# Optimization experiments

Hardware: AMD Instinct MI355X
Metric: run time of the kernel (lower is better)

## Reference

```python
import jax, jax.numpy as jnp
import numpy as np

BLOCK = 64
# Standard NF4 codebook (bitsandbytes), 16 quantile-based values in [-1, 1].
NF4_CODEBOOK = jnp.array([
    -1.0, -0.6961928009986877, -0.5250730514526367, -0.39491748809814453,
    -0.28444138169288635, -0.18477343022823334, -0.09105003625154495, 0.0,
    0.07958029955625534, 0.16093020141124725, 0.24611230194568634,
    0.33791524171829224, 0.44070982933044434, 0.5626170039176941,
    0.6848514676094055, 1.0], dtype=jnp.float32)


def dequantize_nf4(codes, absmax, shape):
    # codes: int array of 4-bit indices (unpacked), absmax: one scale per BLOCK.
    vals = NF4_CODEBOOK[codes.reshape(-1)]              # [N]
    vals = vals.reshape(-1, BLOCK) * absmax[:, None]    # blockwise rescale
    return vals.reshape(shape)


def setup_inputs() -> dict:
    key = jax.random.key(0)
    k1, k2, k3, k4, k5 = jax.random.split(key, 5)
    B, S, D_IN, D_OUT = 4, 2048, 4096, 4096
    x = jax.random.normal(k1, (B, S, D_IN), dtype=jnp.float32)
    w_codes = jax.random.randint(k2, (D_OUT, D_IN), 0, 16, dtype=jnp.int32)
    w_absmax = jax.random.uniform(k3, (D_OUT * D_IN // BLOCK,), dtype=jnp.float32)
    b_codes = jax.random.randint(k4, (D_OUT,), 0, 16, dtype=jnp.int32)
    b_absmax = jax.random.uniform(k5, (D_OUT // BLOCK,), dtype=jnp.float32)
    return {"x": x, "w_codes": w_codes, "w_absmax": w_absmax,
            "b_codes": b_codes, "b_absmax": b_absmax}


def reference(x, w_codes, w_absmax, b_codes, b_absmax):
    W = dequantize_nf4(w_codes, w_absmax, w_codes.shape)   # [out, in]
    b = dequantize_nf4(b_codes, b_absmax, b_codes.shape)   # [out]
    # F.linear(x, W, b) = x @ W.T + b
    return jnp.einsum('bsd,od->bso', x, W) + b
```

## Files before the change

kernel.cpp:

```cpp
#include <hip/hip_runtime.h>
#include <stdint.h>

typedef __bf16 bf16_t;
typedef __attribute__((ext_vector_type(8))) __bf16 bf16x8;
typedef __attribute__((ext_vector_type(4))) float f32x4;
typedef __attribute__((ext_vector_type(8))) unsigned short ushort8;
typedef __attribute__((ext_vector_type(4))) int int4v;
typedef __attribute__((ext_vector_type(4))) float float4v;

typedef const void __attribute__((address_space(1)))* gptr_t;
typedef void __attribute__((address_space(3)))* lptr_t;

__constant__ float NF4_CB[16] = {
    -1.0f, -0.6961928009986877f, -0.5250730514526367f, -0.39491748809814453f,
    -0.28444138169288635f, -0.18477343022823334f, -0.09105003625154495f, 0.0f,
    0.07958029955625534f, 0.16093020141124725f, 0.24611230194568634f,
    0.33791524171829224f, 0.44070982933044434f, 0.5626170039176941f,
    0.6848514676094055f, 1.0f};

__device__ __forceinline__ unsigned short f32_to_bf16_rne(float f) {
    unsigned int u = __float_as_uint(f);
    u += 0x7FFFu + ((u >> 16) & 1u);
    return (unsigned short)(u >> 16);
}

__global__ void prep_kernel(const int* __restrict__ w_codes,
                            const float* __restrict__ w_absmax,
                            const float* __restrict__ x,
                            const int* __restrict__ b_codes,
                            const float* __restrict__ b_absmax,
                            unsigned short* __restrict__ outW,
                            unsigned short* __restrict__ outA,
                            float* __restrict__ outBias,
                            long w16, long x16, int nbias, long wb, long xb) {
    __shared__ float cb[16];
    if (threadIdx.x < 16) cb[threadIdx.x] = NF4_CB[threadIdx.x];
    __syncthreads();

    long blk = blockIdx.x;
    if (blk < wb) {
        long t = blk * blockDim.x + threadIdx.x;
        if (t >= w16) return;
        long base = t * 16;
        float am = w_absmax[t >> 2];
        int4v c0 = *(const int4v*)(w_codes + base);
        int4v c1 = *(const int4v*)(w_codes + base + 4);
        int4v c2 = *(const int4v*)(w_codes + base + 8);
        int4v c3 = *(const int4v*)(w_codes + base + 12);
        ushort8 v0, v1;
        v0[0] = f32_to_bf16_rne(cb[c0[0]] * am);
        v0[1] = f32_to_bf16_rne(cb[c0[1]] * am);
        v0[2] = f32_to_bf16_rne(cb[c0[2]] * am);
        v0[3] = f32_to_bf16_rne(cb[c0[3]] * am);
        v0[4] = f32_to_bf16_rne(cb[c1[0]] * am);
        v0[5] = f32_to_bf16_rne(cb[c1[1]] * am);
        v0[6] = f32_to_bf16_rne(cb[c1[2]] * am);
        v0[7] = f32_to_bf16_rne(cb[c1[3]] * am);
        v1[0] = f32_to_bf16_rne(cb[c2[0]] * am);
        v1[1] = f32_to_bf16_rne(cb[c2[1]] * am);
        v1[2] = f32_to_bf16_rne(cb[c2[2]] * am);
        v1[3] = f32_to_bf16_rne(cb[c2[3]] * am);
        v1[4] = f32_to_bf16_rne(cb[c3[0]] * am);
        v1[5] = f32_to_bf16_rne(cb[c3[1]] * am);
        v1[6] = f32_to_bf16_rne(cb[c3[2]] * am);
        v1[7] = f32_to_bf16_rne(cb[c3[3]] * am);
        *(ushort8*)(outW + base) = v0;
        *(ushort8*)(outW + base + 8) = v1;
    } else if (blk < wb + xb) {
        long t = (blk - wb) * blockDim.x + threadIdx.x;
        if (t >= x16) return;
        long base = t * 16;
        float4v f0 = *(const float4v*)(x + base);
        float4v f1 = *(const float4v*)(x + base + 4);
        float4v f2 = *(const float4v*)(x + base + 8);
        float4v f3 = *(const float4v*)(x + base + 12);
        ushort8 v0, v1;
        v0[0] = f32_to_bf16_rne(f0[0]);
        v0[1] = f32_to_bf16_rne(f0[1]);
        v0[2] = f32_to_bf16_rne(f0[2]);
        v0[3] = f32_to_bf16_rne(f0[3]);
        v0[4] = f32_to_bf16_rne(f1[0]);
        v0[5] = f32_to_bf16_rne(f1[1]);
        v0[6] = f32_to_bf16_rne(f1[2]);
        v0[7] = f32_to_bf16_rne(f1[3]);
        v1[0] = f32_to_bf16_rne(f2[0]);
        v1[1] = f32_to_bf16_rne(f2[1]);
        v1[2] = f32_to_bf16_rne(f2[2]);
        v1[3] = f32_to_bf16_rne(f2[3]);
        v1[4] = f32_to_bf16_rne(f3[0]);
        v1[5] = f32_to_bf16_rne(f3[1]);
        v1[6] = f32_to_bf16_rne(f3[2]);
        v1[7] = f32_to_bf16_rne(f3[3]);
        *(ushort8*)(outA + base) = v0;
        *(ushort8*)(outA + base + 8) = v1;
    } else {
        int o = (int)(blk - wb - xb) * blockDim.x + threadIdx.x;
        if (o >= nbias) return;
        outBias[o] = cb[b_codes[o]] * b_absmax[o >> 6];
    }
}

__global__ __launch_bounds__(512, 2) void gemm_bias_kernel_256x256(
        const bf16_t* __restrict__ A, const bf16_t* __restrict__ B,
        const float* __restrict__ bias, float* __restrict__ C,
        int M, int N, int K) {
    __shared__ __align__(16) bf16_t sAB[65536];

    const int t = threadIdx.x;
    const int lane = t & 63;
    const int wave = t >> 6;

    const int nbx = gridDim.x;
    const int nwg = nbx * (int)gridDim.y;
    int flat = (int)blockIdx.y * nbx + (int)blockIdx.x;
    if ((nwg & 7) == 0) flat = (flat & 7) * (nwg >> 3) + (flat >> 3);
    const int tileM = (flat / nbx) * 256;
    const int tileN = (flat % nbx) * 256;

    const int rloc = lane >> 3;
    const int jsw  = (lane & 7) ^ rloc;
    const bf16_t* srcp[8];
#pragma unroll
    for (int j = 0; j < 8; ++j) {
        int c = wave * 8 + j;
        int isB = c >> 5;
        int r = (c & 31) * 8 + rloc;
        const bf16_t* base = isB ? (B + (size_t)(tileN + r) * K)
                                 : (A + (size_t)(tileM + r) * K);
        srcp[j] = base + jsw * 8;
    }
    bf16_t* dst0 = &sAB[wave * 4096 + lane * 8];

    auto stage = [&](int bufsel) {
        bf16_t* d = dst0 + bufsel * 32768;
#pragma unroll
        for (int j = 0; j < 8; ++j) {
            __builtin_amdgcn_global_load_lds((gptr_t)srcp[j],
                                             (lptr_t)(d + j * 512), 16, 0, 0);
            srcp[j] += 64;
        }
    };

    const int wm = wave >> 2;
    const int wn = wave & 3;
    const int la = lane & 15;
    const int jA = lane >> 4;
    const int jj0 = (jA ^ (lane & 7)) * 8;
    const int aoff = (wm * 128 + la) * 64 + jj0;
    const int boff = 16384 + (wn * 64 + la) * 64 + jj0;

    f32x4 acc[8][4] = {};
    const int nt = K >> 6;

    stage(0);
    stage(1);
    asm volatile("s_waitcnt vmcnt(8)" ::: "memory");
    __builtin_amdgcn_s_barrier();
    asm volatile("" ::: "memory");

    for (int kt = 0; kt < nt; ++kt) {
        const int base = (kt & 1) << 15;
#pragma unroll
        for (int kh = 0; kh < 2; ++kh) {
            const int kx = kh << 5;
            bf16x8 a[4], b[4];
#pragma unroll
            for (int i = 0; i < 4; ++i)
                b[i] = *(const bf16x8*)&sAB[((boff + i * 1024) ^ kx) + base];
#pragma unroll
            for (int i = 0; i < 4; ++i)
                a[i] = *(const bf16x8*)&sAB[((aoff + i * 1024) ^ kx) + base];
            __builtin_amdgcn_s_setprio(1);
#pragma unroll
            for (int mi = 0; mi < 4; ++mi)
#pragma unroll
                for (int ni = 0; ni < 4; ++ni)
                    acc[mi][ni] = __builtin_amdgcn_mfma_f32_16x16x32_bf16(
                        a[mi], b[ni], acc[mi][ni], 0, 0, 0);
            __builtin_amdgcn_s_setprio(0);
#pragma unroll
            for (int i = 0; i < 4; ++i)
                a[i] = *(const bf16x8*)&sAB[((aoff + (i + 4) * 1024) ^ kx) + base];
            __builtin_amdgcn_s_setprio(1);
#pragma unroll
            for (int mi = 0; mi < 4; ++mi)
#pragma unroll
                for (int ni = 0; ni < 4; ++ni)
                    acc[mi + 4][ni] = __builtin_amdgcn_mfma_f32_16x16x32_bf16(
                        a[mi], b[ni], acc[mi + 4][ni], 0, 0, 0);
            __builtin_amdgcn_s_setprio(0);
        }
        asm volatile("" ::: "memory");
        __builtin_amdgcn_s_barrier();
        if (kt + 2 < nt) {
            stage(kt & 1);
            asm volatile("s_waitcnt vmcnt(8)" ::: "memory");
        } else {
            asm volatile("s_waitcnt vmcnt(0)" ::: "memory");
        }
        __builtin_amdgcn_s_barrier();
        asm volatile("" ::: "memory");
    }

    const int col0 = tileN + wn * 64 + la;
    const int row0 = tileM + wm * 128 + jA * 4;
    float bv[4];
#pragma unroll
    for (int ni = 0; ni < 4; ++ni) bv[ni] = bias[col0 + ni * 16];
#pragma unroll
    for (int mi = 0; mi < 8; ++mi)
#pragma unroll
        for (int ni = 0; ni < 4; ++ni)
#pragma unroll
            for (int r = 0; r < 4; ++r)
                C[(size_t)(row0 + mi * 16 + r) * N + (col0 + ni * 16)] =
                    acc[mi][ni][r] + bv[ni];
}

__global__ __launch_bounds__(512) void gemm_bias_kernel_256(
        const bf16_t* __restrict__ A, const bf16_t* __restrict__ B,
        const float* __restrict__ bias, float* __restrict__ C,
        int M, int N, int K) {
    __shared__ __align__(16) bf16_t sAB[24576];

    const int t = threadIdx.x;
    const int lane = t & 63;
    const int wave = t >> 6;
    const int tileM = blockIdx.y * 256;
    const int tileN = blockIdx.x * 128;

    const int rloc = lane >> 3;
    const int jsw  = (lane & 7) ^ rloc;
    const bf16_t* srcp[6];
    bf16_t* dstp[6];
#pragma unroll
    for (int j = 0; j < 6; ++j) {
        int c = wave * 6 + j;
        int isB = (c >= 32);
        int r = (isB ? (c - 32) : c) * 8 + rloc;
        const bf16_t* base = isB ? (B + (size_t)(tileN + r) * K)
                                 : (A + (size_t)(tileM + r) * K);
        srcp[j] = base + jsw * 8;
        dstp[j] = &sAB[c * 512 + lane * 8];
    }

    const int wm = wave >> 1;
    const int wn = wave & 1;
    const int la = lane & 15;
    const int jA = lane >> 4;
    const int jj0 = (jA ^ (lane & 7)) * 8;
    const int aoff = (wm * 64 + la) * 64 + jj0;
    const int boff = 16384 + (wn * 64 + la) * 64 + jj0;

    f32x4 acc[4][4] = {};

    for (int kt = 0; kt < K; kt += 64) {
#pragma unroll
        for (int j = 0; j < 6; ++j) {
            __builtin_amdgcn_global_load_lds((gptr_t)(srcp[j]), (lptr_t)(dstp[j]),
                                             16, 0, 0);
            srcp[j] += 64;
        }
        __syncthreads();

#pragma unroll
        for (int kh = 0; kh < 2; ++kh) {
            const int kx = kh * 32;
            bf16x8 a[4], b[4];
#pragma unroll
            for (int i = 0; i < 4; ++i) a[i] = *(const bf16x8*)&sAB[(aoff + i * 1024) ^ kx];
#pragma unroll
            for (int i = 0; i < 4; ++i) b[i] = *(const bf16x8*)&sAB[(boff + i * 1024) ^ kx];
#pragma unroll
            for (int mi = 0; mi < 4; ++mi)
#pragma unroll
                for (int ni = 0; ni < 4; ++ni)
                    acc[mi][ni] = __builtin_amdgcn_mfma_f32_16x16x32_bf16(
                        a[mi], b[ni], acc[mi][ni], 0, 0, 0);
        }
        __syncthreads();
    }

    const int col0 = tileN + wn * 64 + la;
    const int row0 = tileM + wm * 64 + jA * 4;
    float bv[4];
#pragma unroll
    for (int ni = 0; ni < 4; ++ni) bv[ni] = bias[col0 + ni * 16];
#pragma unroll
    for (int mi = 0; mi < 4; ++mi)
#pragma unroll
        for (int ni = 0; ni < 4; ++ni)
#pragma unroll
            for (int r = 0; r < 4; ++r)
                C[(size_t)(row0 + mi * 16 + r) * N + (col0 + ni * 16)] =
                    acc[mi][ni][r] + bv[ni];
}

__global__ void gemm_bias_kernel_128(const bf16_t* __restrict__ A,
                                     const bf16_t* __restrict__ B,
                                     const float* __restrict__ bias,
                                     float* __restrict__ C,
                                     int M, int N, int K) {
    __shared__ __align__(16) bf16_t sAB[16384];
    const int t = threadIdx.x;
    const int lane = t & 63;
    const int wave = t >> 6;
    const int tileM = blockIdx.y * 128;
    const int tileN = blockIdx.x * 128;

    const int rloc = lane >> 3;
    const int jsw  = (lane & 7) ^ rloc;
    const int chunk0 = wave * 8;
    const int isB = chunk0 >> 4;
    const int ci0 = chunk0 & 15;
    const int r0 = ci0 * 8 + rloc;
    const bf16_t* srcp = (isB ? (B + (size_t)(tileN + r0) * K)
                              : (A + (size_t)(tileM + r0) * K)) + jsw * 8;
    bf16_t* dstp = &sAB[isB * 8192 + ci0 * 512 + lane * 8];
    const size_t srcChunkStride = (size_t)8 * K;

    const int wm = wave >> 1;
    const int wn = wave & 1;
    const int la = lane & 15;
    const int jA = lane >> 4;
    const int jj0 = (jA ^ (lane & 7)) * 8;
    const int aoff = (wm * 64 + la) * 64 + jj0;
    const int boff = 8192 + (wn * 64 + la) * 64 + jj0;

    f32x4 acc[4][4] = {};
    for (int kt = 0; kt < K; kt += 64) {
#pragma unroll
        for (int j8 = 0; j8 < 8; ++j8)
            __builtin_amdgcn_global_load_lds((gptr_t)(srcp + j8 * srcChunkStride),
                                             (lptr_t)(dstp + j8 * 512), 16, 0, 0);
        srcp += 64;
        __syncthreads();
#pragma unroll
        for (int kh = 0; kh < 2; ++kh) {
            const int kx = kh * 32;
            bf16x8 a[4], b[4];
#pragma unroll
            for (int i = 0; i < 4; ++i) a[i] = *(const bf16x8*)&sAB[(aoff + i * 1024) ^ kx];
#pragma unroll
            for (int i = 0; i < 4; ++i) b[i] = *(const bf16x8*)&sAB[(boff + i * 1024) ^ kx];
#pragma unroll
            for (int mi = 0; mi < 4; ++mi)
#pragma unroll
                for (int ni = 0; ni < 4; ++ni)
                    acc[mi][ni] = __builtin_amdgcn_mfma_f32_16x16x32_bf16(
                        a[mi], b[ni], acc[mi][ni], 0, 0, 0);
        }
        __syncthreads();
    }
    const int col0 = tileN + wn * 64 + la;
    const int row0 = tileM + wm * 64 + jA * 4;
    float bv[4];
#pragma unroll
    for (int ni = 0; ni < 4; ++ni) bv[ni] = bias[col0 + ni * 16];
#pragma unroll
    for (int mi = 0; mi < 4; ++mi)
#pragma unroll
        for (int ni = 0; ni < 4; ++ni)
#pragma unroll
            for (int r = 0; r < 4; ++r)
                C[(size_t)(row0 + mi * 16 + r) * N + (col0 + ni * 16)] =
                    acc[mi][ni][r] + bv[ni];
}

extern "C" void kernel_launch(void* const* d_in, const int* in_sizes, int n_in,
                              void* d_out, int out_size, void* d_ws, size_t ws_size,
                              hipStream_t stream) {
    const float* x        = (const float*)d_in[0];
    const int*   w_codes  = (const int*)d_in[1];
    const float* w_absmax = (const float*)d_in[2];
    const int*   b_codes  = (const int*)d_in[3];
    const float* b_absmax = (const float*)d_in[4];
    float* out = (float*)d_out;

    const int  D_OUT = in_sizes[3];
    const long WK    = (long)in_sizes[1];
    const int  D_IN  = (int)(WK / D_OUT);
    const long xN    = (long)in_sizes[0];
    const int  M     = (int)(xN / D_IN);
    const int  N = D_OUT, K = D_IN;

    unsigned short* wsW = (unsigned short*)d_ws;
    unsigned short* wsA = wsW + (size_t)N * K;
    float* wsBias = (float*)(wsA + (size_t)M * K);

    long w16 = WK / 16;
    long x16 = xN / 16;
    long wb = (w16 + 255) / 256;
    long xb = (x16 + 255) / 256;
    long bb = (D_OUT + 255) / 256;
    prep_kernel<<<dim3((unsigned)(wb + xb + bb)), dim3(256), 0, stream>>>(
        w_codes, w_absmax, x, b_codes, b_absmax, wsW, wsA, wsBias,
        w16, x16, D_OUT, wb, xb);

    if (M % 256 == 0 && N % 256 == 0 && K % 64 == 0 && K >= 128) {
        gemm_bias_kernel_256x256<<<dim3(N / 256, M / 256), dim3(512), 0, stream>>>(
            (const bf16_t*)wsA, (const bf16_t*)wsW, wsBias, out, M, N, K);
    } else if (M % 256 == 0) {
        gemm_bias_kernel_256<<<dim3(N / 128, M / 256), dim3(512), 0, stream>>>(
            (const bf16_t*)wsA, (const bf16_t*)wsW, wsBias, out, M, N, K);
    } else {
        gemm_bias_kernel_128<<<dim3(N / 128, M / 128), dim3(256), 0, stream>>>(
            (const bf16_t*)wsA, (const bf16_t*)wsW, wsBias, out, M, N, K);
    }
}
```

Baseline: 514.5 us.

## Restructure 256x256 GEMM main loop into four-phase ping-pong with register prefetch

Replaces the per-tile loop (load all fragments, then MFMA, then barrier plus a full stage of global-to-LDS loads) with a four-phase tile body. Each phase issues half of the next tile's global_load_lds, loads the next register fragments from LDS, and runs a 16-MFMA quadrant, with barriers between phases. The first A/B fragments of the next tile are prefetched into registers during the last quadrant. The aim is to hide LDS reads and global loads behind MFMA work. In exchange it uses more barriers and vmcnt(0) waits, needs more registers for the double fragment sets, and now requires K divisible by 128.

```diff
diff --git a/kernel.cpp b/kernel.cpp
--- a/kernel.cpp
+++ b/kernel.cpp
@@ -100,7 +100,64 @@
     }
 }
 
-__global__ __launch_bounds__(512, 2) void gemm_bias_kernel_256x256(
+#define BAR() do { asm volatile("" ::: "memory"); \
+                   __builtin_amdgcn_s_barrier(); \
+                   asm volatile("" ::: "memory"); } while (0)
+#define VM0() asm volatile("s_waitcnt vmcnt(0)" ::: "memory")
+
+#define LOAD_A(dst, i0, BASE) do { \
+  _Pragma("unroll") for (int ii_ = 0; ii_ < 4; ++ii_) \
+    _Pragma("unroll") for (int kh_ = 0; kh_ < 2; ++kh_) \
+      dst[ii_][kh_] = *(const bf16x8*)&sAB[((aoff + ((i0) + ii_) * 1024) ^ (kh_ << 5)) + (BASE)]; \
+} while (0)
+
+#define LOAD_B(dst, n0, BASE) do { \
+  _Pragma("unroll") for (int nn_ = 0; nn_ < 2; ++nn_) \
+    _Pragma("unroll") for (int kh_ = 0; kh_ < 2; ++kh_) \
+      dst[nn_][kh_] = *(const bf16x8*)&sAB[((boff + ((n0) + nn_) * 1024) ^ (kh_ << 5)) + (BASE)]; \
+} while (0)
+
+#define MFMA16(areg, breg, r, c) do { \
+  __builtin_amdgcn_s_setprio(1); \
+  _Pragma("unroll") for (int kh_ = 0; kh_ < 2; ++kh_) \
+    _Pragma("unroll") for (int ii_ = 0; ii_ < 4; ++ii_) \
+      _Pragma("unroll") for (int nn_ = 0; nn_ < 2; ++nn_) \
+        acc[4*(r)+ii_][2*(c)+nn_] = __builtin_amdgcn_mfma_f32_16x16x32_bf16( \
+            areg[ii_][kh_], breg[nn_][kh_], acc[4*(r)+ii_][2*(c)+nn_], 0, 0, 0); \
+  __builtin_amdgcn_s_setprio(0); \
+} while (0)
+
+#define STAGE4(j0, BSEL) do { \
+  bf16_t* d_ = dst0 + (BSEL) * 32768; \
+  _Pragma("unroll") for (int j_ = 0; j_ < 4; ++j_) { \
+    __builtin_amdgcn_global_load_lds((gptr_t)srcp[(j0) + j_], \
+                                     (lptr_t)(d_ + ((j0) + j_) * 512), 16, 0, 0); \
+    srcp[(j0) + j_] += 64; \
+  } \
+} while (0)
+
+#define TILE_BODY(CURB, NXTB, NSEL, B03, B12, DOST, DOPF) do { \
+   \
+  BAR(); \
+  if (DOST) STAGE4(0, NSEL); \
+  LOAD_B(B12, 2, CURB); \
+  MFMA16(aS0, B03, 0, 0); \
+   \
+  BAR(); \
+  if (DOST) STAGE4(4, NSEL); \
+  LOAD_A(aS1, 4, CURB); \
+  MFMA16(aS0, B12, 0, 1); \
+   \
+  VM0(); \
+  BAR(); \
+  MFMA16(aS1, B12, 1, 1); \
+   \
+  BAR(); \
+  if (DOPF) { LOAD_A(aS0, 0, NXTB); LOAD_B(B12, 0, NXTB); } \
+  MFMA16(aS1, B03, 1, 0); \
+} while (0)
+
+__global__ __launch_bounds__(512, 2) void gemm_bias_kernel_256x256_fp(
         const bf16_t* __restrict__ A, const bf16_t* __restrict__ B,
         const float* __restrict__ bias, float* __restrict__ C,
         int M, int N, int K) {
@@ -131,16 +188,6 @@
     }
     bf16_t* dst0 = &sAB[wave * 4096 + lane * 8];
 
-    auto stage = [&](int bufsel) {
-        bf16_t* d = dst0 + bufsel * 32768;
-#pragma unroll
-        for (int j = 0; j < 8; ++j) {
-            __builtin_amdgcn_global_load_lds((gptr_t)srcp[j],
-                                             (lptr_t)(d + j * 512), 16, 0, 0);
-            srcp[j] += 64;
-        }
-    };
-
     const int wm = wave >> 2;
     const int wn = wave & 3;
     const int la = lane & 15;
@@ -150,56 +197,24 @@
     const int boff = 16384 + (wn * 64 + la) * 64 + jj0;
 
     f32x4 acc[8][4] = {};
+    bf16x8 aS0[4][2], aS1[4][2], bX[2][2], bY[2][2];
     const int nt = K >> 6;
 
-    stage(0);
-    stage(1);
-    asm volatile("s_waitcnt vmcnt(8)" ::: "memory");
-    __builtin_amdgcn_s_barrier();
-    asm volatile("" ::: "memory");
-
-    for (int kt = 0; kt < nt; ++kt) {
-        const int base = (kt & 1) << 15;
-#pragma unroll
-        for (int kh = 0; kh < 2; ++kh) {
-            const int kx = kh << 5;
-            bf16x8 a[4], b[4];
-#pragma unroll
-            for (int i = 0; i < 4; ++i)
-                b[i] = *(const bf16x8*)&sAB[((boff + i * 1024) ^ kx) + base];
-#pragma unroll
-            for (int i = 0; i < 4; ++i)
-                a[i] = *(const bf16x8*)&sAB[((aoff + i * 1024) ^ kx) + base];
-            __builtin_amdgcn_s_setprio(1);
-#pragma unroll
-            for (int mi = 0; mi < 4; ++mi)
-#pragma unroll
-                for (int ni = 0; ni < 4; ++ni)
-                    acc[mi][ni] = __builtin_amdgcn_mfma_f32_16x16x32_bf16(
-                        a[mi], b[ni], acc[mi][ni], 0, 0, 0);
-            __builtin_amdgcn_s_setprio(0);
-#pragma unroll
-            for (int i = 0; i < 4; ++i)
-                a[i] = *(const bf16x8*)&sAB[((aoff + (i + 4) * 1024) ^ kx) + base];
-            __builtin_amdgcn_s_setprio(1);
-#pragma unroll
-            for (int mi = 0; mi < 4; ++mi)
-#pragma unroll
-                for (int ni = 0; ni < 4; ++ni)
-                    acc[mi + 4][ni] = __builtin_amdgcn_mfma_f32_16x16x32_bf16(
-                        a[mi], b[ni], acc[mi + 4][ni], 0, 0, 0);
-            __builtin_amdgcn_s_setprio(0);
-        }
-        asm volatile("" ::: "memory");
-        __builtin_amdgcn_s_barrier();
-        if (kt + 2 < nt) {
-            stage(kt & 1);
-            asm volatile("s_waitcnt vmcnt(8)" ::: "memory");
-        } else {
-            asm volatile("s_waitcnt vmcnt(0)" ::: "memory");
-        }
-        __builtin_amdgcn_s_barrier();
-        asm volatile("" ::: "memory");
+#pragma unroll
+    for (int j = 0; j < 8; ++j) {
+        __builtin_amdgcn_global_load_lds((gptr_t)srcp[j], (lptr_t)(dst0 + j * 512),
+                                         16, 0, 0);
+        srcp[j] += 64;
+    }
+    VM0();
+    BAR();
+    LOAD_A(aS0, 0, 0);
+    LOAD_B(bX, 0, 0);
+
+    for (int kt = 0; kt < nt; kt += 2) {
+        TILE_BODY(0, 32768, 1, bX, bY, true, true);
+        const bool more = (kt + 2 < nt);
+        TILE_BODY(32768, 0, 0, bY, bX, more, more);
     }
 
     const int col0 = tileN + wn * 64 + la;
@@ -397,8 +412,8 @@
         w_codes, w_absmax, x, b_codes, b_absmax, wsW, wsA, wsBias,
         w16, x16, D_OUT, wb, xb);
 
-    if (M % 256 == 0 && N % 256 == 0 && K % 64 == 0 && K >= 128) {
-        gemm_bias_kernel_256x256<<<dim3(N / 256, M / 256), dim3(512), 0, stream>>>(
+    if (M % 256 == 0 && N % 256 == 0 && K % 128 == 0) {
+        gemm_bias_kernel_256x256_fp<<<dim3(N / 256, M / 256), dim3(512), 0, stream>>>(
             (const bf16_t*)wsA, (const bf16_t*)wsW, wsBias, out, M, N, K);
     } else if (M % 256 == 0) {
         gemm_bias_kernel_256<<<dim3(N / 128, M / 256), dim3(512), 0, stream>>>(
```

Result: slower. 626.7 us (+21.8%).
